# Optimization experiments

Hardware: AMD Instinct MI355X
Metric: run time of the kernel (lower is better)

Reference implementation:

```python
import jax, jax.numpy as jnp
import numpy as np

N, E, D_IN, HID, D_OUT, MAX_DEG = 30000, 480000, 128, 128, 128, 48


def setup_inputs() -> dict:
    key = jax.random.key(0)
    ks = jax.random.split(key, 8)
    input_matrix = jax.random.normal(ks[0], (N, D_IN), jnp.float32)
    edge_src_idxs = jnp.sort(jax.random.randint(ks[1], (E,), 0, N))
    edge_trg_idxs = jax.random.randint(ks[2], (E,), 0, N)
    s = 1.0 / np.sqrt(HID)  # pytorch LSTM init bound
    W_ih = jax.random.uniform(ks[3], (4 * HID, D_IN), jnp.float32, -s, s)
    W_hh = jax.random.uniform(ks[4], (4 * HID, HID), jnp.float32, -s, s)
    b_ih = jax.random.uniform(ks[5], (4 * HID,), jnp.float32, -s, s)
    b_hh = jax.random.uniform(ks[6], (4 * HID,), jnp.float32, -s, s)
    xb = np.sqrt(6.0 / (D_IN + HID + D_OUT))  # xavier uniform
    W_out = jax.random.uniform(ks[7], (D_IN + HID, D_OUT), jnp.float32, -xb, xb)
    return {
        "input_matrix": input_matrix,
        "W_ih": W_ih, "W_hh": W_hh, "b_ih": b_ih, "b_hh": b_hh,
        "W_out": W_out,
        "edge_src_idxs": edge_src_idxs,
        "edge_trg_idxs": edge_trg_idxs,
        "max_deg": MAX_DEG,
    }


def _lstm_last(dense, mask, W_ih, W_hh, b):
    # dense: [N, T, d], mask: [N, T] -> final hidden state at last valid step, [N, H]
    H = W_hh.shape[1]

    def step(carry, xs):
        h, c = carry
        x_t, m_t = xs  # [N, d], [N]
        gates = x_t @ W_ih.T + h @ W_hh.T + b  # [N, 4H], pytorch gate order i,f,g,o
        i, f, g, o = jnp.split(gates, 4, axis=-1)
        c2 = jax.nn.sigmoid(f) * c + jax.nn.sigmoid(i) * jnp.tanh(g)
        h2 = jax.nn.sigmoid(o) * jnp.tanh(c2)
        m = m_t[:, None]
        return (jnp.where(m, h2, h), jnp.where(m, c2, c)), None

    h0 = jnp.zeros((dense.shape[0], H), dense.dtype)
    (h, _), _ = jax.lax.scan(step, (h0, h0), (dense.transpose(1, 0, 2), mask.T))
    return h


def reference(input_matrix, W_ih, W_hh, b_ih, b_hh, W_out,
              edge_src_idxs, edge_trg_idxs, max_deg):
    n, d = input_matrix.shape
    e = edge_src_idxs.shape[0]
    neighbors = input_matrix[edge_trg_idxs]  # [E, d] gather
    # edge_src_idxs is sorted: position of each edge within its source group
    counts = jax.ops.segment_sum(jnp.ones((e,), jnp.int32), edge_src_idxs,
                                 num_segments=n)
    starts = jnp.cumsum(counts) - counts  # exclusive cumsum
    pos = jnp.arange(e) - starts[edge_src_idxs]  # [E]
    # pad ragged neighbor sequences into [N, max_deg, d] (overflow dropped)
    dense = jnp.zeros((n, max_deg, d), input_matrix.dtype).at[edge_src_idxs, pos].set(neighbors)
    mask = jnp.zeros((n, max_deg), bool).at[edge_src_idxs, pos].set(True)
    agg = _lstm_last(dense, mask, W_ih, W_hh, b_ih + b_hh)  # [N, H]; zeros for isolated nodes
    return jnp.concatenate([input_matrix, agg], axis=1) @ W_out
```

## Files before the change

### kernel.cpp

```cpp
#include <hip/hip_runtime.h>

#define NN 30000
#define NE 480000
#define NG 512
#define MAXD 48
#define BATCH 32
#define NB 938
#define HPAD 144
#define NGB 469

typedef __attribute__((ext_vector_type(8))) short short8;
typedef __attribute__((ext_vector_type(4))) short s16x4;
typedef __attribute__((ext_vector_type(4))) float f32x4;
typedef __attribute__((ext_vector_type(4))) int i32x4;

#define L2E 1.44269504089f
#define L2E2 2.88539008178f

static __device__ __forceinline__ short f2bs(float f) {
  unsigned u = __builtin_bit_cast(unsigned, f);
  u = (u + 0x7fffu + ((u >> 16) & 1u)) >> 16;
  return (short)u;
}
static __device__ __forceinline__ void gl_lds16(const short* g, short* l) {
  __builtin_amdgcn_global_load_lds(
      (const __attribute__((address_space(1))) void*)g,
      (__attribute__((address_space(3))) void*)l, 16, 0, 0);
}

#define PIN_AGPR(w_) asm("" : "+a"(w_))

#define EDGE_BLKS 1875
__global__ void k_edges_wcvt(const int* __restrict__ src, int* __restrict__ starts,
                             int* __restrict__ ends,
                             const float* __restrict__ W_ih,
                             const float* __restrict__ W_hh,
                             const float* __restrict__ Wout,
                             short* __restrict__ wih_s, short* __restrict__ whh_s,
                             short* __restrict__ wout_s) {
  const int b = blockIdx.x, tid = threadIdx.x;
  if (b < EDGE_BLKS) {
    int e = b * 256 + tid;
    if (e >= NE) return;
    int s = src[e];
    if (e == 0 || src[e - 1] != s) starts[s] = e;
    if (e == NE - 1 || src[e + 1] != s) ends[s] = e + 1;
    return;
  }
  const int f = b - EDGE_BLKS;
  const int wv = tid >> 6, lq = (tid >> 4) & 3, lc = tid & 15;
  if (f < 64) {
    const float* W = (f < 32) ? W_ih : W_hh;
    short* dst = (f < 32) ? wih_s : whh_s;
    const int ff = f & 31;
    const int g = ff >> 3, db = (ff >> 2) & 1, kt = ff & 3;
    const float s = (g == 2) ? L2E2 : L2E;
    const float* p = &W[(g * 128 + wv * 32 + db * 16 + lc) * 128 + kt * 32 + lq * 8];
    f32x4 a = *(const f32x4*)p;
    f32x4 c = *(const f32x4*)(p + 4);
    short8 w;
    w[0] = f2bs(a[0] * s); w[1] = f2bs(a[1] * s); w[2] = f2bs(a[2] * s); w[3] = f2bs(a[3] * s);
    w[4] = f2bs(c[0] * s); w[5] = f2bs(c[1] * s); w[6] = f2bs(c[2] * s); w[7] = f2bs(c[3] * s);
    *(short8*)&dst[(ff * 256 + tid) * 8] = w;
  } else {
    const int fo = f - 64;
    const int db = fo >> 3, kt = fo & 7;
    short8 w;
#pragma unroll
    for (int jj = 0; jj < 8; ++jj)
      w[jj] = f2bs(Wout[(kt * 32 + lq * 8 + jj) * 128 + wv * 32 + db * 16 + lc]);
    *(short8*)&wout_s[(fo * 256 + tid) * 8] = w;
  }
}

__global__ void k_nbr_hist(const int* __restrict__ src, const int* __restrict__ trg,
                           const int* __restrict__ starts, const int* __restrict__ ends,
                           int* __restrict__ nbr, int* __restrict__ ghist) {
  __shared__ int h[MAXD + 1];
  const int tid = threadIdx.x;
  if (tid <= MAXD) h[tid] = 0;
  __syncthreads();
  int e = blockIdx.x * 256 + tid;
  if (e < NE) {
    int s = src[e];
    int pos = e - starts[s];
    if (pos < MAXD) nbr[s * MAXD + pos] = trg[e];
  }
  if (e < NN) {
    int c = ends[e] - starts[e]; c = c > MAXD ? MAXD : c;
    atomicAdd(&h[c], 1);
  }
  __syncthreads();
  if (tid <= MAXD && h[tid] > 0) atomicAdd(&ghist[tid], h[tid]);
}

__global__ void k_scat2(const int* __restrict__ starts, const int* __restrict__ ends,
                        const int* __restrict__ ghist, int* __restrict__ gclaim,
                        int* __restrict__ order) {
  __shared__ int lh[MAXD + 1];
  __shared__ int lbase[MAXD + 1];
  __shared__ int sbase[MAXD + 1];
  const int tid = threadIdx.x;
  if (tid <= MAXD) lh[tid] = 0;
  __syncthreads();
  int n = blockIdx.x * 256 + tid;
  int c = 0, rank = 0;
  if (n < NN) {
    c = ends[n] - starts[n]; c = c > MAXD ? MAXD : c;
    rank = atomicAdd(&lh[c], 1);
  }
  if (tid == 0) {
    int tot = 0;
    for (int b = MAXD; b >= 0; --b) { sbase[b] = tot; tot += ghist[b]; }
  }
  __syncthreads();
  if (tid <= MAXD && lh[tid] > 0)
    lbase[tid] = sbase[tid] + atomicAdd(&gclaim[tid], lh[tid]);
  __syncthreads();
  if (n < NN) order[lbase[c] + rank] = n;
}

__global__ __launch_bounds__(256)
__attribute__((amdgpu_waves_per_eu(2, 2))) void k_proj(
    const float* __restrict__ x, const short* __restrict__ wih_s,
    const float* __restrict__ b_ih, const float* __restrict__ b_hh,
    short* __restrict__ proj) {
  __shared__ __align__(16) short xs[64 * HPAD];
  const int tid = threadIdx.x;
  const int wv = tid >> 6, lane = tid & 63, lq = lane >> 4, lc = lane & 15;
  const int base = blockIdx.x * 64;

  for (int idx4 = tid; idx4 < 64 * 32; idx4 += 256) {
    int row = idx4 >> 5, k4 = (idx4 & 31) << 2;
    f32x4 v = (f32x4){0.f, 0.f, 0.f, 0.f};
    if (base + row < NN) v = *(const f32x4*)&x[(base + row) * 128 + k4];
    s16x4 p; p[0] = f2bs(v[0]); p[1] = f2bs(v[1]); p[2] = f2bs(v[2]); p[3] = f2bs(v[3]);
    *(s16x4*)&xs[row * HPAD + k4] = p;
  }
  const short8* wihv = (const short8*)wih_s;
  short8 wfrag[4][2][4];
#pragma unroll
  for (int g = 0; g < 4; ++g)
#pragma unroll
    for (int db = 0; db < 2; ++db)
#pragma unroll
      for (int kt = 0; kt < 4; ++kt) {
        short8 w = wihv[(g * 8 + db * 4 + kt) * 256 + tid];
        PIN_AGPR(w);
        wfrag[g][db][kt] = w;
      }
  float bias_v[4][2];
#pragma unroll
  for (int g = 0; g < 4; ++g)
#pragma unroll
    for (int db = 0; db < 2; ++db) {
      int j = g * 128 + wv * 32 + db * 16 + lc;
      bias_v[g][db] = (b_ih[j] + b_hh[j]) * ((g == 2) ? L2E2 : L2E);
    }
  __syncthreads();

#pragma unroll
  for (int mt = 0; mt < 4; ++mt) {
    short8 afrag[4];
#pragma unroll
    for (int kt = 0; kt < 4; ++kt)
      afrag[kt] = *(const short8*)&xs[(mt * 16 + lc) * HPAD + kt * 32 + lq * 8];
    f32x4 acc[4][2];
#pragma unroll
    for (int g = 0; g < 4; ++g)
#pragma unroll
      for (int db = 0; db < 2; ++db) {
        float b = bias_v[g][db];
        acc[g][db] = (f32x4){b, b, b, b};
#pragma unroll
        for (int kt = 0; kt < 4; ++kt)
          acc[g][db] = __builtin_amdgcn_mfma_f32_16x16x32_bf16(
              afrag[kt], wfrag[g][db][kt], acc[g][db], 0, 0, 0);
      }
#pragma unroll
    for (int r = 0; r < 4; ++r) {
      int row = base + mt * 16 + lq * 4 + r;
      if (row < NN) {
        short8 w;
        w[0] = f2bs(acc[0][0][r]); w[1] = f2bs(acc[0][1][r]);
        w[2] = f2bs(acc[1][0][r]); w[3] = f2bs(acc[1][1][r]);
        w[4] = f2bs(acc[2][0][r]); w[5] = f2bs(acc[2][1][r]);
        w[6] = f2bs(acc[3][0][r]); w[7] = f2bs(acc[3][1][r]);
        *(short8*)&proj[row * NG + (wv * 16 + lc) * 8] = w;
      }
    }
  }
}

__global__ __launch_bounds__(256)
__attribute__((amdgpu_waves_per_eu(2, 2))) void k_lstm(
    const short* __restrict__ whh_s, const short* __restrict__ proj,
    const int* __restrict__ order, const int* __restrict__ starts,
    const int* __restrict__ ends, const int* __restrict__ nbr,
    short* __restrict__ agg) {
  __shared__ __align__(16) short h_s[2][BATCH * HPAD];
  __shared__ __align__(16) short pbuf[4][8][64 * 8];
  __shared__ unsigned short nbr_s[BATCH][MAXD];
  __shared__ int nodes_s[BATCH];
  __shared__ int cnts_s[BATCH];

  const int tid = threadIdx.x;
  const int wv = tid >> 6, lane = tid & 63, lq = lane >> 4, lc = lane & 15;

  const short8* whhv = (const short8*)whh_s;
  short8 wfrag[4][2][4];
#pragma unroll
  for (int g = 0; g < 4; ++g)
#pragma unroll
    for (int db = 0; db < 2; ++db)
#pragma unroll
      for (int kt = 0; kt < 4; ++kt) {
        short8 w = whhv[(g * 8 + db * 4 + kt) * 256 + tid];
        PIN_AGPR(w);
        wfrag[g][db][kt] = w;
      }

  const int batch = blockIdx.x;
  if (tid < BATCH) {
    int gidx = batch * BATCH + tid;
    int node = 0, c = 0;
    if (gidx < NN) {
      node = order[gidx];
      c = ends[node] - starts[node]; c = c > MAXD ? MAXD : c;
    }
    nodes_s[tid] = node;
    cnts_s[tid] = c;
  }
  __syncthreads();
  for (int idx = tid; idx < BATCH * HPAD / 2; idx += 256)
    ((int*)h_s[0])[idx] = 0;
  for (int idx = tid; idx < BATCH * MAXD; idx += 256) {
    int m = idx / MAXD, p = idx - m * MAXD;
    nbr_s[m][p] = (unsigned short)nbr[nodes_s[m] * MAXD + p];
  }
  __syncthreads();
  const int T = cnts_s[0];

  int cp[2];
#pragma unroll
  for (int mt = 0; mt < 2; ++mt) {
    int p = 0;
#pragma unroll
    for (int r = 0; r < 4; ++r) p |= cnts_s[mt * 16 + lq * 4 + r] << (r * 8);
    cp[mt] = p;
  }

  float c_v[2][2][4];
  s16x4 hvp[2][2];
#pragma unroll
  for (int mt = 0; mt < 2; ++mt)
#pragma unroll
    for (int db = 0; db < 2; ++db) {
#pragma unroll
      for (int r = 0; r < 4; ++r) c_v[mt][db][r] = 0.0f;
      hvp[mt][db] = (s16x4){0, 0, 0, 0};
    }

  const int pcol = (wv * 16 + lc) * 8;
  if (T > 0) {
#pragma unroll
    for (int mt = 0; mt < 2; ++mt)
#pragma unroll
      for (int r = 0; r < 4; ++r) {
        int m = mt * 16 + lq * 4 + r;
        int nb_i = (0 < ((cp[mt] >> (r * 8)) & 255)) ? (int)nbr_s[m][0] : 0;
        gl_lds16(&proj[nb_i * NG + pcol], &pbuf[wv][mt * 4 + r][0]);
      }
  }

  for (int t = 0; t < T; ++t) {
    __syncthreads();
    const short* hb = h_s[t & 1];
    short* hw = h_s[(t + 1) & 1];
    const int tn = t + 1;
    const int ts = tn < MAXD ? tn : 0;
#pragma unroll
    for (int mt = 0; mt < 2; ++mt) {
      i32x4 pvi[4];
#pragma unroll
      for (int r = 0; r < 4; ++r)
        pvi[r] = *(const i32x4*)&pbuf[wv][mt * 4 + r][lane * 8];
      f32x4 acc[4][2];
#pragma unroll
      for (int g = 0; g < 4; ++g)
#pragma unroll
        for (int r = 0; r < 4; ++r) {
          unsigned u = (unsigned)pvi[r][g];
          acc[g][0][r] = __builtin_bit_cast(float, u << 16);
          acc[g][1][r] = __builtin_bit_cast(float, u & 0xffff0000u);
        }
      __builtin_amdgcn_sched_barrier(0);
      if (tn < T) {
#pragma unroll
        for (int r = 0; r < 4; ++r) {
          int m = mt * 16 + lq * 4 + r;
          int nb_i = (tn < ((cp[mt] >> (r * 8)) & 255)) ? (int)nbr_s[m][ts] : 0;
          gl_lds16(&proj[nb_i * NG + pcol], &pbuf[wv][mt * 4 + r][0]);
        }
      }
      __builtin_amdgcn_sched_barrier(0);
      short8 afrag[4];
#pragma unroll
      for (int kt = 0; kt < 4; ++kt)
        afrag[kt] = *(const short8*)&hb[(mt * 16 + lc) * HPAD + kt * 32 + lq * 8];
#pragma unroll
      for (int g = 0; g < 4; ++g)
#pragma unroll
        for (int db = 0; db < 2; ++db)
#pragma unroll
          for (int kt = 0; kt < 4; ++kt)
            acc[g][db] = __builtin_amdgcn_mfma_f32_16x16x32_bf16(
                afrag[kt], wfrag[g][db][kt], acc[g][db], 0, 0, 0);
#pragma unroll
      for (int db = 0; db < 2; ++db)
#pragma unroll
        for (int r = 0; r < 4; ++r) {
          float Ei = __builtin_amdgcn_exp2f(-acc[0][db][r]);
          float Eg = __builtin_amdgcn_exp2f(fminf(acc[2][db][r], 125.f));
          float ig = (Eg - 1.f) *
                     __builtin_amdgcn_rcpf((1.f + Ei) * (1.f + Eg));
          float fv = __builtin_amdgcn_rcpf(
              1.f + __builtin_amdgcn_exp2f(-acc[1][db][r]));
          float c2 = fv * c_v[mt][db][r] + ig;
          float Eo = __builtin_amdgcn_exp2f(-acc[3][db][r]);
          float Ec = __builtin_amdgcn_exp2f(fminf(c2 * L2E2, 125.f));
          float h2 = (Ec - 1.f) *
                     __builtin_amdgcn_rcpf((1.f + Eo) * (1.f + Ec));
          if (t < ((cp[mt] >> (r * 8)) & 255)) {
            c_v[mt][db][r] = c2;
            hvp[mt][db][r] = f2bs(h2);
          }
        }
#pragma unroll
      for (int db = 0; db < 2; ++db)
#pragma unroll
        for (int r = 0; r < 4; ++r)
          hw[(mt * 16 + lq * 4 + r) * HPAD + wv * 32 + db * 16 + lc] =
              hvp[mt][db][r];
    }
  }
  __syncthreads();
  const short* hf = h_s[T & 1];
  for (int idx = tid; idx < BATCH * 128; idx += 256) {
    int m = idx >> 7, d = idx & 127;
    if (batch * BATCH + m < NN) agg[nodes_s[m] * 128 + d] = hf[m * HPAD + d];
  }
}

__global__ __launch_bounds__(256, 2) void k_out(
    const float* __restrict__ x, const short* __restrict__ agg,
    const short* __restrict__ wout_s, float* __restrict__ out) {
  __shared__ __align__(16) short xs[64 * 272];
  const int tid = threadIdx.x;
  const int wv = tid >> 6, lane = tid & 63, lq = lane >> 4, lc = lane & 15;
  const int base = blockIdx.x * 64;

  for (int idx4 = tid; idx4 < 64 * 32; idx4 += 256) {
    int row = idx4 >> 5, k4 = (idx4 & 31) << 2;
    f32x4 v = (f32x4){0.f, 0.f, 0.f, 0.f};
    if (base + row < NN) v = *(const f32x4*)&x[(base + row) * 128 + k4];
    s16x4 p; p[0] = f2bs(v[0]); p[1] = f2bs(v[1]); p[2] = f2bs(v[2]); p[3] = f2bs(v[3]);
    *(s16x4*)&xs[row * 272 + k4] = p;
    s16x4 a = (s16x4){0, 0, 0, 0};
    if (base + row < NN) a = *(const s16x4*)&agg[(base + row) * 128 + k4];
    *(s16x4*)&xs[row * 272 + 128 + k4] = a;
  }
  const short8* wov = (const short8*)wout_s;
  short8 wf[2][8];
#pragma unroll
  for (int db = 0; db < 2; ++db)
#pragma unroll
    for (int kt = 0; kt < 8; ++kt)
      wf[db][kt] = wov[(db * 8 + kt) * 256 + tid];
  __syncthreads();

#pragma unroll
  for (int mt = 0; mt < 4; ++mt) {
    short8 afrag[8];
#pragma unroll
    for (int kt = 0; kt < 8; ++kt)
      afrag[kt] = *(const short8*)&xs[(mt * 16 + lc) * 272 + kt * 32 + lq * 8];
    f32x4 acc[2];
#pragma unroll
    for (int db = 0; db < 2; ++db) {
      acc[db] = (f32x4){0.f, 0.f, 0.f, 0.f};
#pragma unroll
      for (int kt = 0; kt < 8; ++kt)
        acc[db] = __builtin_amdgcn_mfma_f32_16x16x32_bf16(
            afrag[kt], wf[db][kt], acc[db], 0, 0, 0);
    }
#pragma unroll
    for (int db = 0; db < 2; ++db)
#pragma unroll
      for (int r = 0; r < 4; ++r) {
        int row = base + mt * 16 + lq * 4 + r;
        if (row < NN)
          out[row * 128 + wv * 32 + db * 16 + lc] = acc[db][r];
      }
  }
}

extern "C" void kernel_launch(void* const* d_in, const int* in_sizes, int n_in,
                              void* d_out, int out_size, void* d_ws,
                              size_t ws_size, hipStream_t stream) {
  (void)in_sizes; (void)n_in; (void)out_size; (void)ws_size;
  const float* x     = (const float*)d_in[0];
  const float* W_ih  = (const float*)d_in[1];
  const float* W_hh  = (const float*)d_in[2];
  const float* b_ih  = (const float*)d_in[3];
  const float* b_hh  = (const float*)d_in[4];
  const float* W_out = (const float*)d_in[5];
  const int*   esrc  = (const int*)d_in[6];
  const int*   etrg  = (const int*)d_in[7];
  float* out = (float*)d_out;
  char* ws = (char*)d_ws;

  int*   starts = (int*)(ws + 0);
  int*   ends   = (int*)(ws + 120064);
  int*   ghist  = (int*)(ws + 240128);
  int*   gclaim = (int*)(ws + 240384);
  int*   order  = (int*)(ws + 240640);
  int*   nbr    = (int*)(ws + 360704);
  short* proj   = (short*)(ws + 6120704);
  short* agg    = (short*)(ws + 36840704);
  short* wih_s  = (short*)(ws + 44520704);
  short* whh_s  = (short*)(ws + 44651776);
  short* wout_s = (short*)(ws + 44782848);

  (void)hipMemsetAsync(d_ws, 0, 240640, stream);

  k_edges_wcvt<<<EDGE_BLKS + 80, 256, 0, stream>>>(esrc, starts, ends, W_ih,
                                                   W_hh, W_out, wih_s, whh_s,
                                                   wout_s);
  k_nbr_hist<<<1875, 256, 0, stream>>>(esrc, etrg, starts, ends, nbr, ghist);
  k_scat2<<<118, 256, 0, stream>>>(starts, ends, ghist, gclaim, order);
  k_proj <<<NGB, 256, 0, stream>>>(x, wih_s, b_ih, b_hh, proj);
  k_lstm <<<NB, 256, 0, stream>>>(whh_s, proj, order, starts, ends, nbr, agg);
  k_out  <<<NGB, 256, 0, stream>>>(x, agg, wout_s, out);
}
```

Measured before the change: 250.0 us.

## Fuse output projection into LSTM kernel and use packed bf16 conversion

The final concat-and-W_out matmul now runs at the end of the LSTM kernel, reusing pbuf shared memory to stage the x row and final h for each 32-node batch. This drops the agg round-trip through global memory and one kernel launch. Output rows are scattered by node id. It also swaps manual bf16 rounding for the v_cvt_pk_bf16_f32 instruction in the proj and staging paths. The cost is higher register pressure in k_lstm, since W_out fragments are pinned to AGPRs, plus a tail phase per block.

```diff
diff --git a/kernel.cpp b/kernel.cpp
--- a/kernel.cpp
+++ b/kernel.cpp
@@ -8,6 +8,7 @@
 #define NB 938
 #define HPAD 144
 #define NGB 469
+#define XTS 272
 
 typedef __attribute__((ext_vector_type(8))) short short8;
 typedef __attribute__((ext_vector_type(4))) short s16x4;
@@ -21,6 +22,11 @@
   unsigned u = __builtin_bit_cast(unsigned, f);
   u = (u + 0x7fffu + ((u >> 16) & 1u)) >> 16;
   return (short)u;
+}
+static __device__ __forceinline__ unsigned cvtpk(float lo, float hi) {
+  unsigned r;
+  asm("v_cvt_pk_bf16_f32 %0, %1, %2" : "=v"(r) : "v"(lo), "v"(hi));
+  return r;
 }
 static __device__ __forceinline__ void gl_lds16(const short* g, short* l) {
   __builtin_amdgcn_global_load_lds(
@@ -134,8 +140,9 @@
     int row = idx4 >> 5, k4 = (idx4 & 31) << 2;
     f32x4 v = (f32x4){0.f, 0.f, 0.f, 0.f};
     if (base + row < NN) v = *(const f32x4*)&x[(base + row) * 128 + k4];
-    s16x4 p; p[0] = f2bs(v[0]); p[1] = f2bs(v[1]); p[2] = f2bs(v[2]); p[3] = f2bs(v[3]);
-    *(s16x4*)&xs[row * HPAD + k4] = p;
+    int* xr = (int*)&xs[row * HPAD];
+    xr[(k4 >> 1)] = (int)cvtpk(v[0], v[1]);
+    xr[(k4 >> 1) + 1] = (int)cvtpk(v[2], v[3]);
   }
   const short8* wihv = (const short8*)wih_s;
   short8 wfrag[4][2][4];
@@ -181,12 +188,12 @@
     for (int r = 0; r < 4; ++r) {
       int row = base + mt * 16 + lq * 4 + r;
       if (row < NN) {
-        short8 w;
-        w[0] = f2bs(acc[0][0][r]); w[1] = f2bs(acc[0][1][r]);
-        w[2] = f2bs(acc[1][0][r]); w[3] = f2bs(acc[1][1][r]);
-        w[4] = f2bs(acc[2][0][r]); w[5] = f2bs(acc[2][1][r]);
-        w[6] = f2bs(acc[3][0][r]); w[7] = f2bs(acc[3][1][r]);
-        *(short8*)&proj[row * NG + (wv * 16 + lc) * 8] = w;
+        i32x4 w;
+        w[0] = (int)cvtpk(acc[0][0][r], acc[0][1][r]);
+        w[1] = (int)cvtpk(acc[1][0][r], acc[1][1][r]);
+        w[2] = (int)cvtpk(acc[2][0][r], acc[2][1][r]);
+        w[3] = (int)cvtpk(acc[3][0][r], acc[3][1][r]);
+        *(i32x4*)&proj[row * NG + (wv * 16 + lc) * 8] = w;
       }
     }
   }
@@ -197,7 +204,8 @@
     const short* __restrict__ whh_s, const short* __restrict__ proj,
     const int* __restrict__ order, const int* __restrict__ starts,
     const int* __restrict__ ends, const int* __restrict__ nbr,
-    short* __restrict__ agg) {
+    const short* __restrict__ wout_s, const float* __restrict__ x,
+    float* __restrict__ out) {
   __shared__ __align__(16) short h_s[2][BATCH * HPAD];
   __shared__ __align__(16) short pbuf[4][8][64 * 8];
   __shared__ unsigned short nbr_s[BATCH][MAXD];
@@ -345,46 +353,37 @@
     }
   }
   __syncthreads();
+
   const short* hf = h_s[T & 1];
-  for (int idx = tid; idx < BATCH * 128; idx += 256) {
-    int m = idx >> 7, d = idx & 127;
-    if (batch * BATCH + m < NN) agg[nodes_s[m] * 128 + d] = hf[m * HPAD + d];
-  }
-}
-
-__global__ __launch_bounds__(256, 2) void k_out(
-    const float* __restrict__ x, const short* __restrict__ agg,
-    const short* __restrict__ wout_s, float* __restrict__ out) {
-  __shared__ __align__(16) short xs[64 * 272];
-  const int tid = threadIdx.x;
-  const int wv = tid >> 6, lane = tid & 63, lq = lane >> 4, lc = lane & 15;
-  const int base = blockIdx.x * 64;
-
-  for (int idx4 = tid; idx4 < 64 * 32; idx4 += 256) {
-    int row = idx4 >> 5, k4 = (idx4 & 31) << 2;
-    f32x4 v = (f32x4){0.f, 0.f, 0.f, 0.f};
-    if (base + row < NN) v = *(const f32x4*)&x[(base + row) * 128 + k4];
-    s16x4 p; p[0] = f2bs(v[0]); p[1] = f2bs(v[1]); p[2] = f2bs(v[2]); p[3] = f2bs(v[3]);
-    *(s16x4*)&xs[row * 272 + k4] = p;
-    s16x4 a = (s16x4){0, 0, 0, 0};
-    if (base + row < NN) a = *(const s16x4*)&agg[(base + row) * 128 + k4];
-    *(s16x4*)&xs[row * 272 + 128 + k4] = a;
+  short* xt = (short*)pbuf;
+  for (int idx = tid; idx < BATCH * 64; idx += 256) {
+    int m = idx >> 6, d2 = idx & 63;
+    ((int*)xt)[m * (XTS / 2) + 64 + d2] = ((const int*)&hf[m * HPAD])[d2];
+  }
+  for (int idx4 = tid; idx4 < BATCH * 32; idx4 += 256) {
+    int m = idx4 >> 5, k4 = (idx4 & 31) << 2;
+    f32x4 v = *(const f32x4*)&x[nodes_s[m] * 128 + k4];
+    int* xr = (int*)xt + m * (XTS / 2);
+    xr[(k4 >> 1)] = (int)cvtpk(v[0], v[1]);
+    xr[(k4 >> 1) + 1] = (int)cvtpk(v[2], v[3]);
   }
   const short8* wov = (const short8*)wout_s;
   short8 wf[2][8];
 #pragma unroll
   for (int db = 0; db < 2; ++db)
 #pragma unroll
+    for (int kt = 0; kt < 8; ++kt) {
+      short8 w = wov[(db * 8 + kt) * 256 + tid];
+      PIN_AGPR(w);
+      wf[db][kt] = w;
+    }
+  __syncthreads();
+#pragma unroll
+  for (int mt = 0; mt < 2; ++mt) {
+    short8 afrag[8];
+#pragma unroll
     for (int kt = 0; kt < 8; ++kt)
-      wf[db][kt] = wov[(db * 8 + kt) * 256 + tid];
-  __syncthreads();
-
-#pragma unroll
-  for (int mt = 0; mt < 4; ++mt) {
-    short8 afrag[8];
-#pragma unroll
-    for (int kt = 0; kt < 8; ++kt)
-      afrag[kt] = *(const short8*)&xs[(mt * 16 + lc) * 272 + kt * 32 + lq * 8];
+      afrag[kt] = *(const short8*)&xt[(mt * 16 + lc) * XTS + kt * 32 + lq * 8];
     f32x4 acc[2];
 #pragma unroll
     for (int db = 0; db < 2; ++db) {
@@ -398,9 +397,9 @@
     for (int db = 0; db < 2; ++db)
 #pragma unroll
       for (int r = 0; r < 4; ++r) {
-        int row = base + mt * 16 + lq * 4 + r;
-        if (row < NN)
-          out[row * 128 + wv * 32 + db * 16 + lc] = acc[db][r];
+        int m = mt * 16 + lq * 4 + r;
+        if (batch * BATCH + m < NN)
+          out[nodes_s[m] * 128 + wv * 32 + db * 16 + lc] = acc[db][r];
       }
   }
 }
@@ -427,10 +426,9 @@
   int*   order  = (int*)(ws + 240640);
   int*   nbr    = (int*)(ws + 360704);
   short* proj   = (short*)(ws + 6120704);
-  short* agg    = (short*)(ws + 36840704);
-  short* wih_s  = (short*)(ws + 44520704);
-  short* whh_s  = (short*)(ws + 44651776);
-  short* wout_s = (short*)(ws + 44782848);
+  short* wih_s  = (short*)(ws + 36840704);
+  short* whh_s  = (short*)(ws + 36971776);
+  short* wout_s = (short*)(ws + 37102848);
 
   (void)hipMemsetAsync(d_ws, 0, 240640, stream);
 
@@ -440,6 +438,6 @@
   k_nbr_hist<<<1875, 256, 0, stream>>>(esrc, etrg, starts, ends, nbr, ghist);
   k_scat2<<<118, 256, 0, stream>>>(starts, ends, ghist, gclaim, order);
   k_proj <<<NGB, 256, 0, stream>>>(x, wih_s, b_ih, b_hh, proj);
-  k_lstm <<<NB, 256, 0, stream>>>(whh_s, proj, order, starts, ends, nbr, agg);
-  k_out  <<<NGB, 256, 0, stream>>>(x, agg, wout_s, out);
-}
+  k_lstm <<<NB, 256, 0, stream>>>(whh_s, proj, order, starts, ends, nbr,
+                                  wout_s, x, out);
+}
```

Result: faster. 237.2 us (-5.1%).
